# Optimization experiments

Hardware: AMD Instinct MI355X
Metric: run time of the kernel (lower is better)

The kernel has to match this reference:

```python
import jax, jax.numpy as jnp
import numpy as np

DIM = 1024
NUM_HEADS = 16
HEAD_DIM = DIM // NUM_HEADS
SCALE = HEAD_DIM ** -0.5


def setup_inputs() -> dict:
    key = jax.random.key(0)
    k1, k2, k3 = jax.random.split(key, 3)
    x = jax.random.normal(k1, (2, 2048, DIM), dtype=jnp.float32)
    # nn.Linear weights: stored as [out, in]; y = x @ W.T
    w_qkv = jax.random.normal(k2, (3 * DIM, DIM), dtype=jnp.float32) * (DIM ** -0.5)
    w_proj = jax.random.normal(k3, (DIM, DIM), dtype=jnp.float32) * (DIM ** -0.5)
    return {"x": x, "w_qkv": w_qkv, "w_proj": w_proj}


def reference(x, w_qkv, w_proj):
    B, L, D = x.shape
    qkv = jnp.einsum("bld,ed->ble", x, w_qkv)  # [B, L, 3*D]
    qkv = qkv.reshape(B, L, 3, NUM_HEADS, HEAD_DIM).transpose(2, 0, 3, 1, 4)
    q, k, v = qkv[0], qkv[1], qkv[2]  # each [B, H, L, hd]
    attn = jnp.einsum("bhqd,bhkd->bhqk", q, k) * SCALE
    attn = jax.nn.softmax(attn, axis=-1)
    out = jnp.einsum("bhqk,bhkd->bhqd", attn, v)  # [B, H, L, hd]
    out = out.transpose(0, 2, 1, 3).reshape(B, L, D)
    return jnp.einsum("bld,ed->ble", out, w_proj)
```

## Files before the change

### kernel.cpp

```cpp
#include <hip/hip_runtime.h>
#include <math.h>
#include <stdint.h>

#define B_ 2
#define L_ 2048
#define D_ 1024
#define H_ 16
#define HD_ 64
#define QSCALE_ 0.1803368801f

typedef __attribute__((ext_vector_type(8))) short short8;
typedef __attribute__((ext_vector_type(4))) short short4v;
typedef __attribute__((ext_vector_type(4))) float float4v;

#if defined(__has_builtin)
#if __has_builtin(__builtin_amdgcn_exp2f)
#define EXP2F(x) __builtin_amdgcn_exp2f(x)
#endif
#endif
#ifndef EXP2F
#define EXP2F(x) exp2f(x)
#endif

__device__ __forceinline__ short f2bf(float f) {
    union { float f; unsigned u; } x; x.f = f;
    unsigned r = x.u + 0x7fffu + ((x.u >> 16) & 1u);
    return (short)(r >> 16);
}

__device__ __forceinline__ float bf2f(short s) {
    union { unsigned u; float f; } x;
    x.u = ((unsigned)(unsigned short)s) << 16;
    return x.f;
}

__device__ __forceinline__ unsigned fbits(float f) {
    union { float f; unsigned u; } x; x.f = f;
    return x.u;
}

__device__ __forceinline__ unsigned pk_bf_trunc(float a, float b) {
    return __builtin_amdgcn_perm(fbits(b), fbits(a), 0x07060302u);
}

__global__ __launch_bounds__(256) void cvt_all(const float* __restrict__ x,
                                               const float* __restrict__ wqkv,
                                               const float* __restrict__ wproj,
                                               short* __restrict__ xb,
                                               short* __restrict__ wqkvb,
                                               short* __restrict__ wprojb) {
    int i = blockIdx.x * 256 + threadIdx.x;
    const float* in;
    short* out;
    int idx;
    if (i < 1048576)      { in = x;     out = xb;     idx = i; }
    else if (i < 1835008) { in = wqkv;  out = wqkvb;  idx = i - 1048576; }
    else                  { in = wproj; out = wprojb; idx = i - 1835008; }
    float4 v = ((const float4*)in)[idx];
    short4v o;
    o.x = f2bf(v.x); o.y = f2bf(v.y); o.z = f2bf(v.z); o.w = f2bf(v.w);
    ((short4v*)out)[idx] = o;
}

#define LDA_ 40
__global__ __launch_bounds__(512) void gemm_qkv_bf16(const short* __restrict__ A,
                                                     const short* __restrict__ Bm,
                                                     short* __restrict__ Qb,
                                                     short* __restrict__ Kb,
                                                     short* __restrict__ Vb) {
    __shared__ short smem[20480];
    const int tid = threadIdx.x;
    const int w = tid >> 6, l = tid & 63;
    const int lm = l & 15, q = l >> 4;
    const int bid = blockIdx.x;
    const int xcd = bid & 7;
    const int grp = bid >> 3;
    const int n_tile = xcd + 8 * (grp % 3);
    const int m_tile = grp / 3;
    const int m0 = m_tile * 128, n0 = n_tile * 128;
    const int wm = w >> 2, wn = w & 3;

    const int srow = tid >> 2;
    const int sc8  = (tid & 3) * 8;
    const int soff = srow * LDA_ + sc8;
    const short* Ag = A  + (size_t)(m0 + srow) * 1024 + sc8;
    const short* Bg = Bm + (size_t)(n0 + srow) * 1024 + sc8;

    float4v acc[4][2];
#pragma unroll
    for (int mt = 0; mt < 4; ++mt)
#pragma unroll
        for (int nt = 0; nt < 2; ++nt) acc[mt][nt] = (float4v){0.f, 0.f, 0.f, 0.f};

    {
        short8 a0 = *(const short8*)(Ag);
        short8 b0 = *(const short8*)(Bg);
        *(short8*)(smem + soff) = a0;
        *(short8*)(smem + 10240 + soff) = b0;
    }
    short8 ar = *(const short8*)(Ag + 32);
    short8 br = *(const short8*)(Bg + 32);

    for (int t = 0; t < 32; ++t) {
        const int cur = t & 1;
        short* Asc = smem + cur * 5120;
        short* Asn = smem + (1 - cur) * 5120;
        short* Bsc = smem + 10240 + cur * 5120;
        short* Bsn = smem + 10240 + (1 - cur) * 5120;

        __syncthreads();

        if (t < 31) {
            *(short8*)(Asn + soff) = ar;
            *(short8*)(Bsn + soff) = br;
        }
        if (t < 30) {
            const int k0 = (t + 2) * 32;
            ar = *(const short8*)(Ag + k0);
            br = *(const short8*)(Bg + k0);
        }

        short8 af[4], bfr[2];
#pragma unroll
        for (int mt = 0; mt < 4; ++mt)
            af[mt] = *(const short8*)(Asc + (wm * 64 + mt * 16 + lm) * LDA_ + q * 8);
#pragma unroll
        for (int nt = 0; nt < 2; ++nt)
            bfr[nt] = *(const short8*)(Bsc + (wn * 32 + nt * 16 + lm) * LDA_ + q * 8);
#pragma unroll
        for (int mt = 0; mt < 4; ++mt)
#pragma unroll
            for (int nt = 0; nt < 2; ++nt)
                acc[mt][nt] = __builtin_amdgcn_mfma_f32_16x16x32_bf16(af[mt], bfr[nt], acc[mt][nt], 0, 0, 0);
    }

    const int which = n0 >> 10;
    if (which < 2) {
        short* dst = (which == 0) ? Qb : Kb;
        const float sc = (which == 0) ? QSCALE_ : 1.0f;
#pragma unroll
        for (int half = 0; half < 2; ++half) {
            __syncthreads();
            if (wm == half) {
#pragma unroll
                for (int mt = 0; mt < 4; ++mt)
#pragma unroll
                    for (int nt = 0; nt < 2; ++nt)
#pragma unroll
                        for (int r = 0; r < 4; ++r)
                            smem[(mt * 16 + q * 4 + r) * 128 + wn * 32 + nt * 16 + lm] =
                                f2bf(acc[mt][nt][r] * sc);
            }
            __syncthreads();
#pragma unroll
            for (int j = 0; j < 2; ++j) {
                const int x = tid + 512 * j;
                const int row = x >> 4, c = x & 15;
                short8 v = *(const short8*)(smem + row * 128 + c * 8);
                const int m = m0 + half * 64 + row;
                const int b = m >> 11, ll = m & 2047;
                const int n = n0 + c * 8;
                const int hh = (n & 1023) >> 6, d = n & 63;
                *(short8*)(dst + (((size_t)b * H_ + hh) * L_ + ll) * HD_ + d) = v;
            }
        }
    } else {
        const int mbase = m0 + wm * 64;
        const int b = mbase >> 11;
        const int llb = (mbase & 2047);
#pragma unroll
        for (int mt = 0; mt < 4; ++mt) {
            const int ll = llb + (mt >> 1) * 32 + q * 8 + (mt & 1) * 4;
#pragma unroll
            for (int nt = 0; nt < 2; ++nt) {
                const int n = n0 + wn * 32 + nt * 16 + lm;
                const int h = (n & 1023) >> 6, d = n & 63;
                short4v pk;
                pk.x = f2bf(acc[mt][nt][0]); pk.y = f2bf(acc[mt][nt][1]);
                pk.z = f2bf(acc[mt][nt][2]); pk.w = f2bf(acc[mt][nt][3]);
                *(short4v*)(Vb + (((size_t)b * H_ + h) * HD_ + d) * L_ + ll) = pk;
            }
        }
    }
}

__global__ __launch_bounds__(512) void attn_mfma(const short* __restrict__ Qb,
                                                 const short* __restrict__ Kb,
                                                 const short* __restrict__ Vtg,
                                                 short* __restrict__ Op0,
                                                 short* __restrict__ Op1,
                                                 float* __restrict__ Lp0,
                                                 float* __restrict__ Lp1) {
    __shared__ short KV[4 * 4096];

    const int tid = threadIdx.x;
    const int w = tid >> 6, l = tid & 63;
    const int lm = l & 15, q = l >> 4;
    const int bid = blockIdx.x;
    const int xcd = bid & 7;
    const int grp = bid >> 3;
    const int combo = xcd * 8 + (grp >> 3);
    const int bh = combo >> 1;
    const int half = combo & 1;
    const int qt = grp & 7;

    const short* Qg = Qb  + ((size_t)bh * L_ + qt * 256) * HD_;
    const short* Kg = Kb  + ((size_t)bh * L_ + half * 1024) * HD_;
    const short* Vg = Vtg + (size_t)bh * HD_ * L_ + half * 1024;

    short8 qf[2][2];
#pragma unroll
    for (int nq = 0; nq < 2; ++nq)
#pragma unroll
        for (int kh = 0; kh < 2; ++kh)
            qf[nq][kh] = *(const short8*)(Qg + (size_t)(w * 32 + nq * 16 + lm) * HD_ + (kh * 4 + q) * 8);

    const int srow = tid >> 3;
    const int sc   = tid & 7;
    const int koff = srow * 64 + ((sc ^ (srow & 7)) * 8);

    {
        short8 ka = *(const short8*)(Kg + (size_t)srow * 64 + sc * 8);
        short8 va = *(const short8*)(Vg + (size_t)srow * L_ + sc * 8);
        *(short8*)(KV + koff) = ka;
        *(short8*)(KV + 4096 + koff) = va;
    }
    short8 kra = *(const short8*)(Kg + (size_t)(64 + srow) * 64 + sc * 8);
    short8 vra = *(const short8*)(Vg + (size_t)srow * L_ + 64 + sc * 8);

    __syncthreads();

    int offA0[4], offA1[4], offV[2][4];
#pragma unroll
    for (int nt = 0; nt < 4; ++nt) {
        const int arow = nt * 16 + lm;
        offA0[nt] = arow * 64 + ((q ^ (arow & 7)) * 8);
        offA1[nt] = arow * 64 + (((4 + q) ^ (arow & 7)) * 8);
#pragma unroll
        for (int kh = 0; kh < 2; ++kh)
            offV[kh][nt] = arow * 64 + (((kh * 4 + q) ^ (arow & 7)) * 8);
    }

    float4v o[4][2];
#pragma unroll
    for (int mt = 0; mt < 4; ++mt)
#pragma unroll
        for (int nq = 0; nq < 2; ++nq) o[mt][nq] = (float4v){0.f, 0.f, 0.f, 0.f};
    float lsum[2] = {0.f, 0.f};

#pragma unroll 2
    for (int t = 0; t < 16; ++t) {
        const int cur = t & 1;
        short* Kl = KV + cur * 8192;
        short* Vt = Kl + 4096;
        short* Kn = KV + (1 - cur) * 8192;
        short* Vn = Kn + 4096;

        __syncthreads();

        if (t < 15) {
            *(short8*)(Kn + koff) = kra;
            *(short8*)(Vn + koff) = vra;
        }
        if (t < 14) {
            kra = *(const short8*)(Kg + (size_t)((t + 2) * 64 + srow) * 64 + sc * 8);
            vra = *(const short8*)(Vg + (size_t)srow * L_ + (t + 2) * 64 + sc * 8);
        }

        float4v st[4][2];
#pragma unroll
        for (int nt = 0; nt < 4; ++nt) {
            short8 a0 = *(const short8*)(Kl + offA0[nt]);
            short8 a1 = *(const short8*)(Kl + offA1[nt]);
#pragma unroll
            for (int nq = 0; nq < 2; ++nq) {
                float4v z = (float4v){0.f, 0.f, 0.f, 0.f};
                z = __builtin_amdgcn_mfma_f32_16x16x32_bf16(a0, qf[nq][0], z, 0, 0, 0);
                z = __builtin_amdgcn_mfma_f32_16x16x32_bf16(a1, qf[nq][1], z, 0, 0, 0);
                st[nt][nq] = z;
            }
        }

        short8 pb[2][2];
#pragma unroll
        for (int nq = 0; nq < 2; ++nq) {
            float e[4][4];
#pragma unroll
            for (int nt = 0; nt < 4; ++nt) {
                e[nt][0] = EXP2F(st[nt][nq][0]);
                e[nt][1] = EXP2F(st[nt][nq][1]);
                e[nt][2] = EXP2F(st[nt][nq][2]);
                e[nt][3] = EXP2F(st[nt][nq][3]);
                lsum[nq] += (e[nt][0] + e[nt][1]) + (e[nt][2] + e[nt][3]);
            }
            union { short8 s8; unsigned u[4]; } p0, p1;
            p0.u[0] = pk_bf_trunc(e[0][0], e[0][1]);
            p0.u[1] = pk_bf_trunc(e[0][2], e[0][3]);
            p0.u[2] = pk_bf_trunc(e[1][0], e[1][1]);
            p0.u[3] = pk_bf_trunc(e[1][2], e[1][3]);
            p1.u[0] = pk_bf_trunc(e[2][0], e[2][1]);
            p1.u[1] = pk_bf_trunc(e[2][2], e[2][3]);
            p1.u[2] = pk_bf_trunc(e[3][0], e[3][1]);
            p1.u[3] = pk_bf_trunc(e[3][2], e[3][3]);
            pb[0][nq] = p0.s8;
            pb[1][nq] = p1.s8;
        }

#pragma unroll
        for (int kh = 0; kh < 2; ++kh)
#pragma unroll
            for (int mt = 0; mt < 4; ++mt) {
                short8 va = *(const short8*)(Vt + offV[kh][mt]);
#pragma unroll
                for (int nq = 0; nq < 2; ++nq)
                    o[mt][nq] = __builtin_amdgcn_mfma_f32_16x16x32_bf16(va, pb[kh][nq], o[mt][nq], 0, 0, 0);
            }
    }

#pragma unroll
    for (int nq = 0; nq < 2; ++nq) {
        float s = lsum[nq];
        s += __shfl_xor(s, 16);
        s += __shfl_xor(s, 32);
        lsum[nq] = s;
    }
    short* Op = half ? Op1 : Op0;
    float* Lp = half ? Lp1 : Lp0;
    short* OgBase = Op + ((size_t)bh * L_ + qt * 256) * HD_;
#pragma unroll
    for (int nq = 0; nq < 2; ++nq) {
        const int qrow = w * 32 + nq * 16 + lm;
#pragma unroll
        for (int mt = 0; mt < 4; ++mt) {
            short4v pk;
            pk.x = f2bf(o[mt][nq][0]);
            pk.y = f2bf(o[mt][nq][1]);
            pk.z = f2bf(o[mt][nq][2]);
            pk.w = f2bf(o[mt][nq][3]);
            *(short4v*)(OgBase + (size_t)qrow * 64 + mt * 16 + q * 4) = pk;
        }
    }
    if (l < 16) {
        const size_t rbase = (size_t)bh * L_ + qt * 256 + w * 32 + l;
        Lp[rbase]      = lsum[0];
        Lp[rbase + 16] = lsum[1];
    }
}

__global__ __launch_bounds__(256) void combine_o(const short* __restrict__ Op0,
                                                 short* __restrict__ Op1,
                                                 const float* __restrict__ Lp0,
                                                 const float* __restrict__ Lp1) {
    const int i = blockIdx.x * 256 + threadIdx.x;
    const int rg = i >> 3, cg = i & 7;
    const float inv = 1.f / (Lp0[rg] + Lp1[rg]);
    const size_t off = (size_t)rg * 64 + cg * 8;
    short8 a = *(const short8*)(Op0 + off);
    short8 b = *(const short8*)(Op1 + off);
    short8 r;
#pragma unroll
    for (int j = 0; j < 8; ++j)
        r[j] = f2bf((bf2f(a[j]) + bf2f(b[j])) * inv);
    *(short8*)(Op1 + off) = r;
}

__global__ __launch_bounds__(256) void gemm_proj_bf16(const short* __restrict__ Ob,
                                                      const short* __restrict__ Wp,
                                                      float* __restrict__ out) {
    __shared__ short As[2 * 2560];
    __shared__ short Bs[2 * 5120];
    const int tid = threadIdx.x;
    const int w = tid >> 6, l = tid & 63;
    const int lm = l & 15, q = l >> 4;
    const int bid = blockIdx.x;
    const int m0 = (bid >> 3) * 64, n0 = (bid & 7) * 128;
    const int wm = w & 1, wn = w >> 1;
    const int b = m0 >> 11, l0 = m0 & 2047;

    const int srow = tid >> 2;
    const int sc8  = (tid & 3) * 8;
    const int aoff = srow * LDA_ + sc8;
    const int boff0 = aoff;
    const int boff1 = aoff + 64 * LDA_;
    const short* Agb = Ob + (((size_t)b * H_) * L_ + l0 + srow) * HD_;
    const short* Bg  = Wp + (size_t)(n0 + srow) * 1024 + sc8;

    float4v acc[2][4];
#pragma unroll
    for (int mt = 0; mt < 2; ++mt)
#pragma unroll
        for (int nt = 0; nt < 4; ++nt) acc[mt][nt] = (float4v){0.f, 0.f, 0.f, 0.f};

    {
        short8 a0 = *(const short8*)(Agb + sc8);
        short8 b0 = *(const short8*)(Bg);
        short8 b1 = *(const short8*)(Bg + 64 * 1024);
        *(short8*)(As + aoff) = a0;
        *(short8*)(Bs + boff0) = b0;
        *(short8*)(Bs + boff1) = b1;
    }
    short8 arx = *(const short8*)(Agb + 32 + sc8);
    short8 brx0 = *(const short8*)(Bg + 32);
    short8 brx1 = *(const short8*)(Bg + 64 * 1024 + 32);

    for (int t = 0; t < 32; ++t) {
        const int cur = t & 1;
        short* Asc = As + cur * 2560;
        short* Asn = As + (1 - cur) * 2560;
        short* Bsc = Bs + cur * 5120;
        short* Bsn = Bs + (1 - cur) * 5120;

        __syncthreads();

        if (t < 31) {
            *(short8*)(Asn + aoff) = arx;
            *(short8*)(Bsn + boff0) = brx0;
            *(short8*)(Bsn + boff1) = brx1;
        }
        if (t < 30) {
            const int tn = t + 2;
            const int hh = tn >> 1, d = (tn & 1) * 32 + sc8;
            arx  = *(const short8*)(Agb + (size_t)hh * L_ * HD_ + d);
            brx0 = *(const short8*)(Bg + tn * 32);
            brx1 = *(const short8*)(Bg + 64 * 1024 + tn * 32);
        }

        short8 af[2], bfr[4];
#pragma unroll
        for (int mt = 0; mt < 2; ++mt)
            af[mt] = *(const short8*)(Asc + (wm * 32 + mt * 16 + lm) * LDA_ + q * 8);
#pragma unroll
        for (int nt = 0; nt < 4; ++nt)
            bfr[nt] = *(const short8*)(Bsc + (wn * 64 + nt * 16 + lm) * LDA_ + q * 8);
#pragma unroll
        for (int mt = 0; mt < 2; ++mt)
#pragma unroll
            for (int nt = 0; nt < 4; ++nt)
                acc[mt][nt] = __builtin_amdgcn_mfma_f32_16x16x32_bf16(af[mt], bfr[nt], acc[mt][nt], 0, 0, 0);
    }

#pragma unroll
    for (int mt = 0; mt < 2; ++mt)
#pragma unroll
        for (int nt = 0; nt < 4; ++nt)
#pragma unroll
            for (int r = 0; r < 4; ++r) {
                const int m = m0 + wm * 32 + mt * 16 + q * 4 + r;
                const int n = n0 + wn * 64 + nt * 16 + lm;
                out[(size_t)m * 1024 + n] = acc[mt][nt][r];
            }
}

extern "C" void kernel_launch(void* const* d_in, const int* in_sizes, int n_in,
                              void* d_out, int out_size, void* d_ws, size_t ws_size,
                              hipStream_t stream) {
    (void)in_sizes; (void)n_in; (void)out_size; (void)ws_size;
    const float* x      = (const float*)d_in[0];
    const float* w_qkv  = (const float*)d_in[1];
    const float* w_proj = (const float*)d_in[2];

    char* ws = (char*)d_ws;
    short* xb     = (short*)(ws);
    short* wqkvb  = (short*)(ws + (8u  << 20));
    short* wprojb = (short*)(ws + (14u << 20));
    short* Qb     = (short*)(ws + (16u << 20));
    short* Kb     = (short*)(ws + (24u << 20));
    short* Vb     = (short*)(ws + (32u << 20));
    short* Ob     = (short*)(ws + (40u << 20));

    short* Op0 = xb;
    short* Op1 = Ob;
    float* Lp0 = (float*)(ws + (8u << 20));
    float* Lp1 = (float*)(ws + (8u << 20) + (256u << 10));

    cvt_all<<<8192, 256, 0, stream>>>(x, w_qkv, w_proj, xb, wqkvb, wprojb);
    gemm_qkv_bf16 <<<768, 512, 0, stream>>>(xb, wqkvb, Qb, Kb, Vb);
    attn_mfma     <<<512, 512, 0, stream>>>(Qb, Kb, Vb, Op0, Op1, Lp0, Lp1);
    combine_o     <<<2048, 256, 0, stream>>>(Op0, Op1, Lp0, Lp1);
    gemm_proj_bf16<<<512, 256, 0, stream>>>(Ob, wprojb, (float*)d_out);
}
```

Measured before the change: 179.7 us.

## Fuse fp32-to-bf16 conversion into GEMM loads and split-attention combine into projection

Removes the separate conversion kernel by having the QKV and projection GEMMs load fp32 inputs and weights directly and convert to bf16 while staging into shared memory. Also removes the combine_o kernel by folding the two-partial sum and normalisation into the projection GEMM's A-tile load. This cuts two launches and the intermediate bf16 round trips through global memory. In exchange, the GEMMs read twice the bytes per element from fp32 sources and repeat the conversion per tile. The projection also re-reads both partials and the L sums for every N tile.

```diff
diff --git a/kernel.cpp b/kernel.cpp
--- a/kernel.cpp
+++ b/kernel.cpp
@@ -43,31 +43,19 @@
     return __builtin_amdgcn_perm(fbits(b), fbits(a), 0x07060302u);
 }
 
-__global__ __launch_bounds__(256) void cvt_all(const float* __restrict__ x,
-                                               const float* __restrict__ wqkv,
-                                               const float* __restrict__ wproj,
-                                               short* __restrict__ xb,
-                                               short* __restrict__ wqkvb,
-                                               short* __restrict__ wprojb) {
-    int i = blockIdx.x * 256 + threadIdx.x;
-    const float* in;
-    short* out;
-    int idx;
-    if (i < 1048576)      { in = x;     out = xb;     idx = i; }
-    else if (i < 1835008) { in = wqkv;  out = wqkvb;  idx = i - 1048576; }
-    else                  { in = wproj; out = wprojb; idx = i - 1835008; }
-    float4 v = ((const float4*)in)[idx];
-    short4v o;
-    o.x = f2bf(v.x); o.y = f2bf(v.y); o.z = f2bf(v.z); o.w = f2bf(v.w);
-    ((short4v*)out)[idx] = o;
+__device__ __forceinline__ void st_cvt(short* dst, float4 a, float4 b) {
+    short8 r;
+    r[0] = f2bf(a.x); r[1] = f2bf(a.y); r[2] = f2bf(a.z); r[3] = f2bf(a.w);
+    r[4] = f2bf(b.x); r[5] = f2bf(b.y); r[6] = f2bf(b.z); r[7] = f2bf(b.w);
+    *(short8*)dst = r;
 }
 
 #define LDA_ 40
-__global__ __launch_bounds__(512) void gemm_qkv_bf16(const short* __restrict__ A,
-                                                     const short* __restrict__ Bm,
-                                                     short* __restrict__ Qb,
-                                                     short* __restrict__ Kb,
-                                                     short* __restrict__ Vb) {
+__global__ __launch_bounds__(512) void gemm_qkv_f32(const float* __restrict__ A,
+                                                    const float* __restrict__ Bm,
+                                                    short* __restrict__ Qb,
+                                                    short* __restrict__ Kb,
+                                                    short* __restrict__ Vb) {
     __shared__ short smem[20480];
     const int tid = threadIdx.x;
     const int w = tid >> 6, l = tid & 63;
@@ -83,8 +71,8 @@
     const int srow = tid >> 2;
     const int sc8  = (tid & 3) * 8;
     const int soff = srow * LDA_ + sc8;
-    const short* Ag = A  + (size_t)(m0 + srow) * 1024 + sc8;
-    const short* Bg = Bm + (size_t)(n0 + srow) * 1024 + sc8;
+    const float* Ag = A  + (size_t)(m0 + srow) * 1024 + sc8;
+    const float* Bg = Bm + (size_t)(n0 + srow) * 1024 + sc8;
 
     float4v acc[4][2];
 #pragma unroll
@@ -93,13 +81,17 @@
         for (int nt = 0; nt < 2; ++nt) acc[mt][nt] = (float4v){0.f, 0.f, 0.f, 0.f};
 
     {
-        short8 a0 = *(const short8*)(Ag);
-        short8 b0 = *(const short8*)(Bg);
-        *(short8*)(smem + soff) = a0;
-        *(short8*)(smem + 10240 + soff) = b0;
-    }
-    short8 ar = *(const short8*)(Ag + 32);
-    short8 br = *(const short8*)(Bg + 32);
+        float4 a00 = *(const float4*)(Ag);
+        float4 a01 = *(const float4*)(Ag + 4);
+        float4 b00 = *(const float4*)(Bg);
+        float4 b01 = *(const float4*)(Bg + 4);
+        st_cvt(smem + soff, a00, a01);
+        st_cvt(smem + 10240 + soff, b00, b01);
+    }
+    float4 ar0 = *(const float4*)(Ag + 32);
+    float4 ar1 = *(const float4*)(Ag + 36);
+    float4 br0 = *(const float4*)(Bg + 32);
+    float4 br1 = *(const float4*)(Bg + 36);
 
     for (int t = 0; t < 32; ++t) {
         const int cur = t & 1;
@@ -111,13 +103,15 @@
         __syncthreads();
 
         if (t < 31) {
-            *(short8*)(Asn + soff) = ar;
-            *(short8*)(Bsn + soff) = br;
+            st_cvt(Asn + soff, ar0, ar1);
+            st_cvt(Bsn + soff, br0, br1);
         }
         if (t < 30) {
             const int k0 = (t + 2) * 32;
-            ar = *(const short8*)(Ag + k0);
-            br = *(const short8*)(Bg + k0);
+            ar0 = *(const float4*)(Ag + k0);
+            ar1 = *(const float4*)(Ag + k0 + 4);
+            br0 = *(const float4*)(Bg + k0);
+            br1 = *(const float4*)(Bg + k0 + 4);
         }
 
         short8 af[4], bfr[2];
@@ -347,26 +341,12 @@
     }
 }
 
-__global__ __launch_bounds__(256) void combine_o(const short* __restrict__ Op0,
-                                                 short* __restrict__ Op1,
-                                                 const float* __restrict__ Lp0,
-                                                 const float* __restrict__ Lp1) {
-    const int i = blockIdx.x * 256 + threadIdx.x;
-    const int rg = i >> 3, cg = i & 7;
-    const float inv = 1.f / (Lp0[rg] + Lp1[rg]);
-    const size_t off = (size_t)rg * 64 + cg * 8;
-    short8 a = *(const short8*)(Op0 + off);
-    short8 b = *(const short8*)(Op1 + off);
-    short8 r;
-#pragma unroll
-    for (int j = 0; j < 8; ++j)
-        r[j] = f2bf((bf2f(a[j]) + bf2f(b[j])) * inv);
-    *(short8*)(Op1 + off) = r;
-}
-
-__global__ __launch_bounds__(256) void gemm_proj_bf16(const short* __restrict__ Ob,
-                                                      const short* __restrict__ Wp,
-                                                      float* __restrict__ out) {
+__global__ __launch_bounds__(256) void gemm_proj_fused(const short* __restrict__ Op0,
+                                                       const short* __restrict__ Op1,
+                                                       const float* __restrict__ Lp0,
+                                                       const float* __restrict__ Lp1,
+                                                       const float* __restrict__ Wp,
+                                                       float* __restrict__ out) {
     __shared__ short As[2 * 2560];
     __shared__ short Bs[2 * 5120];
     const int tid = threadIdx.x;
@@ -382,8 +362,8 @@
     const int aoff = srow * LDA_ + sc8;
     const int boff0 = aoff;
     const int boff1 = aoff + 64 * LDA_;
-    const short* Agb = Ob + (((size_t)b * H_) * L_ + l0 + srow) * HD_;
-    const short* Bg  = Wp + (size_t)(n0 + srow) * 1024 + sc8;
+    const int arow_g = l0 + srow;
+    const float* Bg = Wp + (size_t)(n0 + srow) * 1024 + sc8;
 
     float4v acc[2][4];
 #pragma unroll
@@ -392,16 +372,36 @@
         for (int nt = 0; nt < 4; ++nt) acc[mt][nt] = (float4v){0.f, 0.f, 0.f, 0.f};
 
     {
-        short8 a0 = *(const short8*)(Agb + sc8);
-        short8 b0 = *(const short8*)(Bg);
-        short8 b1 = *(const short8*)(Bg + 64 * 1024);
-        *(short8*)(As + aoff) = a0;
-        *(short8*)(Bs + boff0) = b0;
-        *(short8*)(Bs + boff1) = b1;
-    }
-    short8 arx = *(const short8*)(Agb + 32 + sc8);
-    short8 brx0 = *(const short8*)(Bg + 32);
-    short8 brx1 = *(const short8*)(Bg + 64 * 1024 + 32);
+        const size_t li = (size_t)(b * H_) * L_ + arow_g;
+        const size_t ai = li * HD_ + sc8;
+        short8 x0 = *(const short8*)(Op0 + ai);
+        short8 x1 = *(const short8*)(Op1 + ai);
+        const float inv = 1.f / (Lp0[li] + Lp1[li]);
+        short8 r;
+#pragma unroll
+        for (int j = 0; j < 8; ++j)
+            r[j] = f2bf((bf2f(x0[j]) + bf2f(x1[j])) * inv);
+        *(short8*)(As + aoff) = r;
+        float4 c0 = *(const float4*)(Bg);
+        float4 c1 = *(const float4*)(Bg + 4);
+        float4 c2 = *(const float4*)(Bg + 64 * 1024);
+        float4 c3 = *(const float4*)(Bg + 64 * 1024 + 4);
+        st_cvt(Bs + boff0, c0, c1);
+        st_cvt(Bs + boff1, c2, c3);
+    }
+    short8 ap0, ap1;
+    float lsA;
+    {
+        const size_t li = (size_t)(b * H_) * L_ + arow_g;
+        const size_t ai = li * HD_ + 32 + sc8;
+        ap0 = *(const short8*)(Op0 + ai);
+        ap1 = *(const short8*)(Op1 + ai);
+        lsA = Lp0[li] + Lp1[li];
+    }
+    float4 bw00 = *(const float4*)(Bg + 32);
+    float4 bw01 = *(const float4*)(Bg + 36);
+    float4 bw10 = *(const float4*)(Bg + 64 * 1024 + 32);
+    float4 bw11 = *(const float4*)(Bg + 64 * 1024 + 36);
 
     for (int t = 0; t < 32; ++t) {
         const int cur = t & 1;
@@ -413,16 +413,27 @@
         __syncthreads();
 
         if (t < 31) {
-            *(short8*)(Asn + aoff) = arx;
-            *(short8*)(Bsn + boff0) = brx0;
-            *(short8*)(Bsn + boff1) = brx1;
+            const float inv = 1.f / lsA;
+            short8 r;
+#pragma unroll
+            for (int j = 0; j < 8; ++j)
+                r[j] = f2bf((bf2f(ap0[j]) + bf2f(ap1[j])) * inv);
+            *(short8*)(Asn + aoff) = r;
+            st_cvt(Bsn + boff0, bw00, bw01);
+            st_cvt(Bsn + boff1, bw10, bw11);
         }
         if (t < 30) {
             const int tn = t + 2;
             const int hh = tn >> 1, d = (tn & 1) * 32 + sc8;
-            arx  = *(const short8*)(Agb + (size_t)hh * L_ * HD_ + d);
-            brx0 = *(const short8*)(Bg + tn * 32);
-            brx1 = *(const short8*)(Bg + 64 * 1024 + tn * 32);
+            const size_t li = (size_t)(b * H_ + hh) * L_ + arow_g;
+            const size_t ai = li * HD_ + d;
+            ap0 = *(const short8*)(Op0 + ai);
+            ap1 = *(const short8*)(Op1 + ai);
+            lsA = Lp0[li] + Lp1[li];
+            bw00 = *(const float4*)(Bg + tn * 32);
+            bw01 = *(const float4*)(Bg + tn * 32 + 4);
+            bw10 = *(const float4*)(Bg + 64 * 1024 + tn * 32);
+            bw11 = *(const float4*)(Bg + 64 * 1024 + tn * 32 + 4);
         }
 
         short8 af[2], bfr[4];
@@ -460,22 +471,15 @@
     const float* w_proj = (const float*)d_in[2];
 
     char* ws = (char*)d_ws;
-    short* xb     = (short*)(ws);
-    short* wqkvb  = (short*)(ws + (8u  << 20));
-    short* wprojb = (short*)(ws + (14u << 20));
+    short* Op0    = (short*)(ws);
+    float* Lp0    = (float*)(ws + (8u  << 20));
+    float* Lp1    = (float*)(ws + (8u  << 20) + (256u << 10));
     short* Qb     = (short*)(ws + (16u << 20));
     short* Kb     = (short*)(ws + (24u << 20));
     short* Vb     = (short*)(ws + (32u << 20));
-    short* Ob     = (short*)(ws + (40u << 20));
-
-    short* Op0 = xb;
-    short* Op1 = Ob;
-    float* Lp0 = (float*)(ws + (8u << 20));
-    float* Lp1 = (float*)(ws + (8u << 20) + (256u << 10));
-
-    cvt_all<<<8192, 256, 0, stream>>>(x, w_qkv, w_proj, xb, wqkvb, wprojb);
-    gemm_qkv_bf16 <<<768, 512, 0, stream>>>(xb, wqkvb, Qb, Kb, Vb);
-    attn_mfma     <<<512, 512, 0, stream>>>(Qb, Kb, Vb, Op0, Op1, Lp0, Lp1);
-    combine_o     <<<2048, 256, 0, stream>>>(Op0, Op1, Lp0, Lp1);
-    gemm_proj_bf16<<<512, 256, 0, stream>>>(Ob, wprojb, (float*)d_out);
-}
+    short* Op1    = (short*)(ws + (40u << 20));
+
+    gemm_qkv_f32   <<<768, 512, 0, stream>>>(x, w_qkv, Qb, Kb, Vb);
+    attn_mfma      <<<512, 512, 0, stream>>>(Qb, Kb, Vb, Op0, Op1, Lp0, Lp1);
+    gemm_proj_fused<<<512, 256, 0, stream>>>(Op0, Op1, Lp0, Lp1, w_proj, (float*)d_out);
+}
```

Result: slower. 190.5 us (+6.0%).

## Fuse split-KV combine into proj GEMM and deepen QKV GEMM K-tile

Applied to the files above, without the earlier changes.

Removes the separate combine_o kernel by having the projection GEMM load both partial attention outputs and their softmax sums, then normalise and convert them while staging the A tile into shared memory. This saves one launch and a full round trip of the combined output through global memory. Separately, the QKV GEMM K-step grows from 32 to 64 with a padded LDS stride of 72, which halves the loop iterations and barriers but roughly doubles shared-memory use per block. The cost is extra A-operand loads and ALU work inside the projection GEMM's main loop.

```diff
diff --git a/kernel.cpp b/kernel.cpp
--- a/kernel.cpp
+++ b/kernel.cpp
@@ -62,13 +62,13 @@
     ((short4v*)out)[idx] = o;
 }
 
-#define LDA_ 40
+#define LDK_ 72
 __global__ __launch_bounds__(512) void gemm_qkv_bf16(const short* __restrict__ A,
                                                      const short* __restrict__ Bm,
                                                      short* __restrict__ Qb,
                                                      short* __restrict__ Kb,
                                                      short* __restrict__ Vb) {
-    __shared__ short smem[20480];
+    __shared__ short smem[36864];
     const int tid = threadIdx.x;
     const int w = tid >> 6, l = tid & 63;
     const int lm = l & 15, q = l >> 4;
@@ -82,7 +82,7 @@
 
     const int srow = tid >> 2;
     const int sc8  = (tid & 3) * 8;
-    const int soff = srow * LDA_ + sc8;
+    const int soff = srow * LDK_ + sc8;
     const short* Ag = A  + (size_t)(m0 + srow) * 1024 + sc8;
     const short* Bg = Bm + (size_t)(n0 + srow) * 1024 + sc8;
 
@@ -93,45 +93,57 @@
         for (int nt = 0; nt < 2; ++nt) acc[mt][nt] = (float4v){0.f, 0.f, 0.f, 0.f};
 
     {
-        short8 a0 = *(const short8*)(Ag);
-        short8 b0 = *(const short8*)(Bg);
-        *(short8*)(smem + soff) = a0;
-        *(short8*)(smem + 10240 + soff) = b0;
-    }
-    short8 ar = *(const short8*)(Ag + 32);
-    short8 br = *(const short8*)(Bg + 32);
-
-    for (int t = 0; t < 32; ++t) {
+        *(short8*)(smem + soff)              = *(const short8*)(Ag);
+        *(short8*)(smem + soff + 32)         = *(const short8*)(Ag + 32);
+        *(short8*)(smem + 18432 + soff)      = *(const short8*)(Bg);
+        *(short8*)(smem + 18432 + soff + 32) = *(const short8*)(Bg + 32);
+    }
+    short8 ar0 = *(const short8*)(Ag + 64);
+    short8 ar1 = *(const short8*)(Ag + 96);
+    short8 br0 = *(const short8*)(Bg + 64);
+    short8 br1 = *(const short8*)(Bg + 96);
+
+    for (int t = 0; t < 16; ++t) {
         const int cur = t & 1;
-        short* Asc = smem + cur * 5120;
-        short* Asn = smem + (1 - cur) * 5120;
-        short* Bsc = smem + 10240 + cur * 5120;
-        short* Bsn = smem + 10240 + (1 - cur) * 5120;
+        short* Asc = smem + cur * 9216;
+        short* Asn = smem + (1 - cur) * 9216;
+        short* Bsc = smem + 18432 + cur * 9216;
+        short* Bsn = smem + 18432 + (1 - cur) * 9216;
 
         __syncthreads();
 
-        if (t < 31) {
-            *(short8*)(Asn + soff) = ar;
-            *(short8*)(Bsn + soff) = br;
-        }
-        if (t < 30) {
-            const int k0 = (t + 2) * 32;
-            ar = *(const short8*)(Ag + k0);
-            br = *(const short8*)(Bg + k0);
-        }
-
-        short8 af[4], bfr[2];
+        if (t < 15) {
+            *(short8*)(Asn + soff)      = ar0;
+            *(short8*)(Asn + soff + 32) = ar1;
+            *(short8*)(Bsn + soff)      = br0;
+            *(short8*)(Bsn + soff + 32) = br1;
+        }
+        if (t < 14) {
+            const int k0 = (t + 2) * 64;
+            ar0 = *(const short8*)(Ag + k0);
+            ar1 = *(const short8*)(Ag + k0 + 32);
+            br0 = *(const short8*)(Bg + k0);
+            br1 = *(const short8*)(Bg + k0 + 32);
+        }
+
+        short8 af[4][2], bfr[2][2];
 #pragma unroll
         for (int mt = 0; mt < 4; ++mt)
-            af[mt] = *(const short8*)(Asc + (wm * 64 + mt * 16 + lm) * LDA_ + q * 8);
+#pragma unroll
+            for (int kk = 0; kk < 2; ++kk)
+                af[mt][kk] = *(const short8*)(Asc + (wm * 64 + mt * 16 + lm) * LDK_ + kk * 32 + q * 8);
 #pragma unroll
         for (int nt = 0; nt < 2; ++nt)
-            bfr[nt] = *(const short8*)(Bsc + (wn * 32 + nt * 16 + lm) * LDA_ + q * 8);
-#pragma unroll
-        for (int mt = 0; mt < 4; ++mt)
-#pragma unroll
-            for (int nt = 0; nt < 2; ++nt)
-                acc[mt][nt] = __builtin_amdgcn_mfma_f32_16x16x32_bf16(af[mt], bfr[nt], acc[mt][nt], 0, 0, 0);
+#pragma unroll
+            for (int kk = 0; kk < 2; ++kk)
+                bfr[nt][kk] = *(const short8*)(Bsc + (wn * 32 + nt * 16 + lm) * LDK_ + kk * 32 + q * 8);
+#pragma unroll
+        for (int kk = 0; kk < 2; ++kk)
+#pragma unroll
+            for (int mt = 0; mt < 4; ++mt)
+#pragma unroll
+                for (int nt = 0; nt < 2; ++nt)
+                    acc[mt][nt] = __builtin_amdgcn_mfma_f32_16x16x32_bf16(af[mt][kk], bfr[nt][kk], acc[mt][nt], 0, 0, 0);
     }
 
     const int which = n0 >> 10;
@@ -347,26 +359,13 @@
     }
 }
 
-__global__ __launch_bounds__(256) void combine_o(const short* __restrict__ Op0,
-                                                 short* __restrict__ Op1,
-                                                 const float* __restrict__ Lp0,
-                                                 const float* __restrict__ Lp1) {
-    const int i = blockIdx.x * 256 + threadIdx.x;
-    const int rg = i >> 3, cg = i & 7;
-    const float inv = 1.f / (Lp0[rg] + Lp1[rg]);
-    const size_t off = (size_t)rg * 64 + cg * 8;
-    short8 a = *(const short8*)(Op0 + off);
-    short8 b = *(const short8*)(Op1 + off);
-    short8 r;
-#pragma unroll
-    for (int j = 0; j < 8; ++j)
-        r[j] = f2bf((bf2f(a[j]) + bf2f(b[j])) * inv);
-    *(short8*)(Op1 + off) = r;
-}
-
-__global__ __launch_bounds__(256) void gemm_proj_bf16(const short* __restrict__ Ob,
-                                                      const short* __restrict__ Wp,
-                                                      float* __restrict__ out) {
+#define LDA_ 40
+__global__ __launch_bounds__(256) void gemm_proj_fused(const short* __restrict__ Op0,
+                                                       const short* __restrict__ Op1,
+                                                       const float* __restrict__ Lp0,
+                                                       const float* __restrict__ Lp1,
+                                                       const short* __restrict__ Wp,
+                                                       float* __restrict__ out) {
     __shared__ short As[2 * 2560];
     __shared__ short Bs[2 * 5120];
     const int tid = threadIdx.x;
@@ -382,8 +381,8 @@
     const int aoff = srow * LDA_ + sc8;
     const int boff0 = aoff;
     const int boff1 = aoff + 64 * LDA_;
-    const short* Agb = Ob + (((size_t)b * H_) * L_ + l0 + srow) * HD_;
-    const short* Bg  = Wp + (size_t)(n0 + srow) * 1024 + sc8;
+    const int arow_g = l0 + srow;
+    const short* Bg = Wp + (size_t)(n0 + srow) * 1024 + sc8;
 
     float4v acc[2][4];
 #pragma unroll
@@ -392,14 +391,28 @@
         for (int nt = 0; nt < 4; ++nt) acc[mt][nt] = (float4v){0.f, 0.f, 0.f, 0.f};
 
     {
-        short8 a0 = *(const short8*)(Agb + sc8);
-        short8 b0 = *(const short8*)(Bg);
-        short8 b1 = *(const short8*)(Bg + 64 * 1024);
-        *(short8*)(As + aoff) = a0;
-        *(short8*)(Bs + boff0) = b0;
-        *(short8*)(Bs + boff1) = b1;
-    }
-    short8 arx = *(const short8*)(Agb + 32 + sc8);
+        const size_t li = (size_t)(b * H_) * L_ + arow_g;
+        const size_t ai = li * HD_ + sc8;
+        short8 x0 = *(const short8*)(Op0 + ai);
+        short8 x1 = *(const short8*)(Op1 + ai);
+        const float inv = 1.f / (Lp0[li] + Lp1[li]);
+        short8 r;
+#pragma unroll
+        for (int j = 0; j < 8; ++j)
+            r[j] = f2bf((bf2f(x0[j]) + bf2f(x1[j])) * inv);
+        *(short8*)(As + aoff) = r;
+        *(short8*)(Bs + boff0) = *(const short8*)(Bg);
+        *(short8*)(Bs + boff1) = *(const short8*)(Bg + 64 * 1024);
+    }
+    short8 ap0, ap1;
+    float lsA;
+    {
+        const size_t li = (size_t)(b * H_) * L_ + arow_g;
+        const size_t ai = li * HD_ + 32 + sc8;
+        ap0 = *(const short8*)(Op0 + ai);
+        ap1 = *(const short8*)(Op1 + ai);
+        lsA = Lp0[li] + Lp1[li];
+    }
     short8 brx0 = *(const short8*)(Bg + 32);
     short8 brx1 = *(const short8*)(Bg + 64 * 1024 + 32);
 
@@ -413,14 +426,23 @@
         __syncthreads();
 
         if (t < 31) {
-            *(short8*)(Asn + aoff) = arx;
+            const float inv = 1.f / lsA;
+            short8 r;
+#pragma unroll
+            for (int j = 0; j < 8; ++j)
+                r[j] = f2bf((bf2f(ap0[j]) + bf2f(ap1[j])) * inv);
+            *(short8*)(Asn + aoff) = r;
             *(short8*)(Bsn + boff0) = brx0;
             *(short8*)(Bsn + boff1) = brx1;
         }
         if (t < 30) {
             const int tn = t + 2;
             const int hh = tn >> 1, d = (tn & 1) * 32 + sc8;
-            arx  = *(const short8*)(Agb + (size_t)hh * L_ * HD_ + d);
+            const size_t li = (size_t)(b * H_ + hh) * L_ + arow_g;
+            const size_t ai = li * HD_ + d;
+            ap0 = *(const short8*)(Op0 + ai);
+            ap1 = *(const short8*)(Op1 + ai);
+            lsA = Lp0[li] + Lp1[li];
             brx0 = *(const short8*)(Bg + tn * 32);
             brx1 = *(const short8*)(Bg + 64 * 1024 + tn * 32);
         }
@@ -466,16 +488,14 @@
     short* Qb     = (short*)(ws + (16u << 20));
     short* Kb     = (short*)(ws + (24u << 20));
     short* Vb     = (short*)(ws + (32u << 20));
-    short* Ob     = (short*)(ws + (40u << 20));
+    short* Op1    = (short*)(ws + (40u << 20));
 
     short* Op0 = xb;
-    short* Op1 = Ob;
     float* Lp0 = (float*)(ws + (8u << 20));
     float* Lp1 = (float*)(ws + (8u << 20) + (256u << 10));
 
-    cvt_all<<<8192, 256, 0, stream>>>(x, w_qkv, w_proj, xb, wqkvb, wprojb);
-    gemm_qkv_bf16 <<<768, 512, 0, stream>>>(xb, wqkvb, Qb, Kb, Vb);
-    attn_mfma     <<<512, 512, 0, stream>>>(Qb, Kb, Vb, Op0, Op1, Lp0, Lp1);
-    combine_o     <<<2048, 256, 0, stream>>>(Op0, Op1, Lp0, Lp1);
-    gemm_proj_bf16<<<512, 256, 0, stream>>>(Ob, wprojb, (float*)d_out);
-}
+    cvt_all        <<<8192, 256, 0, stream>>>(x, w_qkv, w_proj, xb, wqkvb, wprojb);
+    gemm_qkv_bf16  <<<768, 512, 0, stream>>>(xb, wqkvb, Qb, Kb, Vb);
+    attn_mfma      <<<512, 512, 0, stream>>>(Qb, Kb, Vb, Op0, Op1, Lp0, Lp1);
+    gemm_proj_fused<<<512, 256, 0, stream>>>(Op0, Op1, Lp0, Lp1, wprojb, (float*)d_out);
+}
```

New measurement: 178.4 us. No clear change (-0.7%).
